# Kernel tuning notes

Measured on AMD Instinct MI355X. Metric: run time of the kernel, lower is better.

The kernel has to match this reference:

```python
import jax, jax.numpy as jnp
import numpy as np

N_NODES = 100000
N_EDGES = 500000
D_IN = 128
D_HID = 256
D_OUT = 1


def mish(x):
    # x * tanh(softplus(x))
    return x * jnp.tanh(jax.nn.softplus(x))


def setup_inputs() -> dict:
    key = jax.random.key(0)
    k1, k2, k3, k4, k5, k6 = jax.random.split(key, 6)
    z = jax.random.normal(k1, (N_NODES, D_IN), dtype=jnp.float32)
    edge = jax.random.randint(k2, (2, N_EDGES), 0, N_NODES, dtype=jnp.int64)
    # PyTorch Linear default init: U(-1/sqrt(fan_in), 1/sqrt(fan_in))
    s1 = 1.0 / np.sqrt(D_IN)
    s2 = 1.0 / np.sqrt(D_HID)
    W1 = jax.random.uniform(k3, (D_HID, D_IN), minval=-s1, maxval=s1, dtype=jnp.float32)
    b1 = jax.random.uniform(k4, (D_HID,), minval=-s1, maxval=s1, dtype=jnp.float32)
    W2 = jax.random.uniform(k5, (D_OUT, D_HID), minval=-s2, maxval=s2, dtype=jnp.float32)
    b2 = jax.random.uniform(k6, (D_OUT,), minval=-s2, maxval=s2, dtype=jnp.float32)
    return {"z": z, "edge": edge, "W1": W1, "b1": b1, "W2": W2, "b2": b2}


def reference(z, edge, W1, b1, W2, b2):
    # gather node pairs and elementwise product: [E, D_IN]
    x = z[edge[0]] * z[edge[1]]
    # fc1 + mish (dropout is identity in eval mode)
    h = mish(jnp.einsum('ed,hd->eh', x, W1) + b1)
    # fc2 + sigmoid -> [E, 1]
    logits = jnp.einsum('eh,oh->eo', h, W2) + b2
    return jax.nn.sigmoid(logits)
```

## Files before the change

kernel.cpp:

```cpp
#include <hip/hip_runtime.h>
#include <hip/hip_bf16.h>


#define N_EDGES 500000
#define D_IN    128
#define D_HID   256
#define M_TILE  32
#define NTILES  (N_EDGES / M_TILE)
#define LDS_STRIDE 136
#define GRID    1024

typedef __bf16 bf16x8 __attribute__((ext_vector_type(8)));
typedef float  f32x16 __attribute__((ext_vector_type(16)));
typedef float  f32x2  __attribute__((ext_vector_type(2)));

union F4H { float4 v; f32x2 h[2]; };

__device__ __forceinline__ unsigned int pkbf(f32x2 q) {
    union { __hip_bfloat162 b; unsigned int u; } c;
    c.b = __float22bfloat162_rn(make_float2(q.x, q.y));
    return c.u;
}

__device__ __forceinline__ f32x2 mish2(f32x2 x) {
    f32x2 xc = {fminf(x.x, 20.0f), fminf(x.y, 20.0f)};
    f32x2 E  = {__expf(xc.x), __expf(xc.y)};
    f32x2 num = E * (E + 2.0f);
    f32x2 den = num + 2.0f;
    f32x2 r  = {__builtin_amdgcn_rcpf(den.x), __builtin_amdgcn_rcpf(den.y)};
    return x * num * r;
}

__global__ __launch_bounds__(512, 2)
void edge_decoder_kernel(const float* __restrict__ z,
                         const int*   __restrict__ edge,
                         const float* __restrict__ W1,
                         const float* __restrict__ b1,
                         const float* __restrict__ W2,
                         const float* __restrict__ b2,
                         float*       __restrict__ out) {
    __shared__ ushort xbuf[2][M_TILE * LDS_STRIDE];
    __shared__ float  lpart[2][8][M_TILE];

    const int t    = threadIdx.x;
    const int wave = t >> 6;
    const int lane = t & 63;
    const int half = lane >> 5;
    const int col  = lane & 31;

    bf16x8 afragW[8];
    {
        const float* wrow = W1 + (size_t)(wave * 32 + col) * D_IN;
        #pragma unroll
        for (int kk = 0; kk < 8; ++kk) {
            const float* wp = wrow + kk * 16 + half * 8;
            F4H w0{*reinterpret_cast<const float4*>(wp)};
            F4H w1{*reinterpret_cast<const float4*>(wp + 4)};
            union { unsigned int u[4]; bf16x8 v; } o;
            o.u[0] = pkbf(w0.h[0]); o.u[1] = pkbf(w0.h[1]);
            o.u[2] = pkbf(w1.h[0]); o.u[3] = pkbf(w1.h[1]);
            afragW[kk] = o.v;
        }
    }
    float b1c[16], w2f[16];
    #pragma unroll
    for (int r = 0; r < 16; ++r) {
        const int n = wave * 32 + (r & 3) + 8 * (r >> 2) + 4 * half;
        b1c[r] = b1[n];
        w2f[r] = W2[n];
    }
    const float b2f = b2[0];

    const int s_slot = t >> 4;
    const int cch    = t & 15;

    int tile = blockIdx.x;
    float4 a0, a1, c0, c1;
    {
        const int e = tile * M_TILE + s_slot;
        const int u = edge[e], v = edge[N_EDGES + e];
        const float* zu = z + (size_t)u * D_IN + cch * 8;
        const float* zv = z + (size_t)v * D_IN + cch * 8;
        a0 = *reinterpret_cast<const float4*>(zu);
        a1 = *reinterpret_cast<const float4*>(zu + 4);
        c0 = *reinterpret_cast<const float4*>(zv);
        c1 = *reinterpret_cast<const float4*>(zv + 4);
    }
    int u_n, v_n;
    {
        const int t1 = min(tile + GRID, NTILES - 1);
        const int e1 = t1 * M_TILE + s_slot;
        u_n = edge[e1]; v_n = edge[N_EDGES + e1];
    }

    int  p = 0;
    bool have_prev = false;
    int  prev_base = 0;

    for (; tile < NTILES; tile += GRID) {
        {
            F4H A0{a0}, A1{a1}, C0{c0}, C1{c1};
            *reinterpret_cast<uint4*>(&xbuf[p][s_slot * LDS_STRIDE + cch * 8]) =
                make_uint4(pkbf(A0.h[0] * C0.h[0]), pkbf(A0.h[1] * C0.h[1]),
                           pkbf(A1.h[0] * C1.h[0]), pkbf(A1.h[1] * C1.h[1]));
        }
        __syncthreads();

        {
            const float* zu = z + (size_t)u_n * D_IN + cch * 8;
            const float* zv = z + (size_t)v_n * D_IN + cch * 8;
            a0 = *reinterpret_cast<const float4*>(zu);
            a1 = *reinterpret_cast<const float4*>(zu + 4);
            c0 = *reinterpret_cast<const float4*>(zv);
            c1 = *reinterpret_cast<const float4*>(zv + 4);
        }
        {
            const int t2 = min(tile + 2 * GRID, NTILES - 1);
            const int e2 = t2 * M_TILE + s_slot;
            u_n = edge[e2]; v_n = edge[N_EDGES + e2];
        }

        if (have_prev && t < M_TILE) {
            const int pp = p ^ 1;
            float logit = b2f;
            #pragma unroll
            for (int w = 0; w < 8; ++w) logit += lpart[pp][w][t];
            out[prev_base + t] = __builtin_amdgcn_rcpf(1.0f + __expf(-logit));
        }

        f32x16 acc;
        #pragma unroll
        for (int r = 0; r < 16; ++r) acc[r] = b1c[r];

        #pragma unroll
        for (int kk = 0; kk < 8; ++kk) {
            bf16x8 bx = *reinterpret_cast<const bf16x8*>(
                &xbuf[p][col * LDS_STRIDE + kk * 16 + half * 8]);
            acc = __builtin_amdgcn_mfma_f32_32x32x16_bf16(afragW[kk], bx, acc, 0, 0, 0);
        }

        float s = 0.f;
        #pragma unroll
        for (int r = 0; r < 16; r += 2) {
            f32x2 h = {acc[r], acc[r + 1]};
            f32x2 m = mish2(h);
            s = fmaf(m.x, w2f[r], s);
            s = fmaf(m.y, w2f[r + 1], s);
        }
        s += __shfl_xor(s, 32);
        if (lane < 32) lpart[p][wave][col] = s;

        have_prev = true;
        prev_base = tile * M_TILE;
        p ^= 1;
    }

    __syncthreads();
    if (have_prev && t < M_TILE) {
        const int pp = p ^ 1;
        float logit = b2f;
        #pragma unroll
        for (int w = 0; w < 8; ++w) logit += lpart[pp][w][t];
        out[prev_base + t] = __builtin_amdgcn_rcpf(1.0f + __expf(-logit));
    }
}

extern "C" void kernel_launch(void* const* d_in, const int* in_sizes, int n_in,
                              void* d_out, int out_size, void* d_ws, size_t ws_size,
                              hipStream_t stream) {
    const float* z    = (const float*)d_in[0];
    const int*   edge = (const int*)d_in[1];
    const float* W1   = (const float*)d_in[2];
    const float* b1   = (const float*)d_in[3];
    const float* W2   = (const float*)d_in[4];
    const float* b2   = (const float*)d_in[5];
    float* out = (float*)d_out;

    edge_decoder_kernel<<<dim3(GRID), dim3(512), 0, stream>>>(z, edge, W1, b1, W2, b2, out);
}
```

Before: 180.0 us.

## Pre-convert z to bf16 and restructure decoder into barrier-free per-wave tiles

Adds a pre-pass that converts the node feature table z to bf16 in the workspace, which halves the bytes fetched by the random gathers. The main kernel now gives each wave a whole 32-edge tile and computes all 256 hidden units itself, using W1 fragments staged in LDS with b1 folded in as an extra K-slice. This removes the block-wide __syncthreads and the LDS reduction of partial logits. The cost is an extra kernel launch, a full pass over z on every call, 8x more LDS reads of W1 per tile, and a fallback to the old kernel when the workspace is too small.

```diff
diff --git a/kernel.cpp b/kernel.cpp
--- a/kernel.cpp
+++ b/kernel.cpp
@@ -2,16 +2,17 @@
 #include <hip/hip_bf16.h>
 
 
+#define N_NODES 100000
 #define N_EDGES 500000
 #define D_IN    128
 #define D_HID   256
-#define M_TILE  32
-#define NTILES  (N_EDGES / M_TILE)
-#define LDS_STRIDE 136
-#define GRID    1024
+#define NTILES  (N_EDGES / 32)
+#define GRID    512
+#define NWAVES  (GRID * 4)
 
 typedef __bf16 bf16x8 __attribute__((ext_vector_type(8)));
 typedef float  f32x16 __attribute__((ext_vector_type(16)));
+typedef float  f32x4  __attribute__((ext_vector_type(4)));
 typedef float  f32x2  __attribute__((ext_vector_type(2)));
 
 union F4H { float4 v; f32x2 h[2]; };
@@ -21,33 +22,183 @@
     c.b = __float22bfloat162_rn(make_float2(q.x, q.y));
     return c.u;
 }
-
-__device__ __forceinline__ f32x2 mish2(f32x2 x) {
-    f32x2 xc = {fminf(x.x, 20.0f), fminf(x.y, 20.0f)};
-    f32x2 E  = {__expf(xc.x), __expf(xc.y)};
-    f32x2 num = E * (E + 2.0f);
-    f32x2 den = num + 2.0f;
-    f32x2 r  = {__builtin_amdgcn_rcpf(den.x), __builtin_amdgcn_rcpf(den.y)};
-    return x * num * r;
-}
-
-__global__ __launch_bounds__(512, 2)
-void edge_decoder_kernel(const float* __restrict__ z,
-                         const int*   __restrict__ edge,
-                         const float* __restrict__ W1,
-                         const float* __restrict__ b1,
-                         const float* __restrict__ W2,
-                         const float* __restrict__ b2,
-                         float*       __restrict__ out) {
-    __shared__ ushort xbuf[2][M_TILE * LDS_STRIDE];
-    __shared__ float  lpart[2][8][M_TILE];
+__device__ __forceinline__ unsigned short f2bf(float f) {
+    union { float f; unsigned int u; } c; c.f = f;
+    return (unsigned short)((c.u + 0x7fffu + ((c.u >> 16) & 1u)) >> 16);
+}
+__device__ __forceinline__ float bflo(unsigned int w) {
+    union { unsigned int u; float f; } c; c.u = w << 16; return c.f;
+}
+__device__ __forceinline__ float bfhi(unsigned int w) {
+    union { unsigned int u; float f; } c; c.u = w & 0xffff0000u; return c.f;
+}
+
+__device__ __forceinline__ float mish_f(float x) {
+    float xc  = fminf(x, 20.0f);
+    float E   = __expf(xc);
+    float num = E * (E + 2.0f);
+    return x * num * __builtin_amdgcn_rcpf(num + 2.0f);
+}
+
+__global__ __launch_bounds__(256)
+void z_to_bf16(const float* __restrict__ z, ushort* __restrict__ zb) {
+    const int i = (blockIdx.x * 256 + threadIdx.x) * 8;
+    F4H a{*reinterpret_cast<const float4*>(z + i)};
+    F4H b{*reinterpret_cast<const float4*>(z + i + 4)};
+    *reinterpret_cast<uint4*>(zb + i) =
+        make_uint4(pkbf(a.h[0]), pkbf(a.h[1]), pkbf(b.h[0]), pkbf(b.h[1]));
+}
+
+__global__ __launch_bounds__(256, 2)
+void edge_decoder_nobar(const ushort* __restrict__ zb,
+                        const int*    __restrict__ edge,
+                        const float*  __restrict__ W1,
+                        const float*  __restrict__ b1,
+                        const float*  __restrict__ W2,
+                        const float*  __restrict__ b2,
+                        float*        __restrict__ out) {
+    __shared__ ushort ldsA[8 * 9 * 64 * 8];
+    __shared__ float  ldsW2[D_HID];
 
     const int t    = threadIdx.x;
     const int wave = t >> 6;
     const int lane = t & 63;
+    const int ecol = lane & 31;
     const int half = lane >> 5;
-    const int col  = lane & 31;
-
+
+    ldsW2[t] = W2[t];
+    for (int c = t; c < 8 * 9 * 64; c += 256) {
+        const int ln = c & 63, mtkk = c >> 6;
+        const int mt = mtkk / 9, kk = mtkk - mt * 9;
+        const int m = mt * 32 + (ln & 31), hf = ln >> 5;
+        union { unsigned int u[4]; uint4 q; } o;
+        if (kk < 8) {
+            const float* wp = W1 + (size_t)m * D_IN + kk * 16 + hf * 8;
+            F4H w0{*reinterpret_cast<const float4*>(wp)};
+            F4H w1{*reinterpret_cast<const float4*>(wp + 4)};
+            o.u[0] = pkbf(w0.h[0]); o.u[1] = pkbf(w0.h[1]);
+            o.u[2] = pkbf(w1.h[0]); o.u[3] = pkbf(w1.h[1]);
+        } else {
+            o.u[0] = o.u[1] = o.u[2] = o.u[3] = 0u;
+            if (hf == 0) o.u[0] = (unsigned int)f2bf(b1[m]);
+        }
+        *reinterpret_cast<uint4*>(&ldsA[c * 8]) = o.q;
+    }
+    __syncthreads();
+
+    const float b2f = b2[0];
+
+    bf16x8 bfr8;
+    {
+        union { unsigned short s[8]; bf16x8 v; } u;
+        #pragma unroll
+        for (int j = 0; j < 8; ++j) u.s[j] = 0;
+        if (half == 0) u.s[0] = 0x3F80;
+        bfr8 = u.v;
+    }
+
+    int T = blockIdx.x * 4 + wave;
+    if (T >= NTILES) return;
+
+    uint4 su[8], sv[8];
+    {
+        const int e = T * 32 + ecol;
+        const int u = edge[e], v = edge[N_EDGES + e];
+        const ushort* ru = zb + (size_t)u * D_IN + half * 8;
+        const ushort* rv = zb + (size_t)v * D_IN + half * 8;
+        #pragma unroll
+        for (int kk = 0; kk < 8; ++kk) {
+            su[kk] = *reinterpret_cast<const uint4*>(ru + kk * 16);
+            sv[kk] = *reinterpret_cast<const uint4*>(rv + kk * 16);
+        }
+    }
+    int eun = 0, evn = 0;
+    {
+        const int Tn = T + NWAVES;
+        if (Tn < NTILES) {
+            const int e = Tn * 32 + ecol;
+            eun = edge[e]; evn = edge[N_EDGES + e];
+        }
+    }
+
+    while (true) {
+        bf16x8 bfr[8];
+        #pragma unroll
+        for (int kk = 0; kk < 8; ++kk) {
+            unsigned int uu[4] = {su[kk].x, su[kk].y, su[kk].z, su[kk].w};
+            unsigned int vv[4] = {sv[kk].x, sv[kk].y, sv[kk].z, sv[kk].w};
+            union { unsigned int u[4]; bf16x8 v; } o;
+            #pragma unroll
+            for (int j = 0; j < 4; ++j) {
+                f32x2 fu = {bflo(uu[j]), bfhi(uu[j])};
+                f32x2 fv = {bflo(vv[j]), bfhi(vv[j])};
+                o.u[j] = pkbf(fu * fv);
+            }
+            bfr[kk] = o.v;
+        }
+
+        const int Tn = T + NWAVES;
+        const bool hn = Tn < NTILES;
+        if (hn) {
+            const ushort* ru = zb + (size_t)eun * D_IN + half * 8;
+            const ushort* rv = zb + (size_t)evn * D_IN + half * 8;
+            #pragma unroll
+            for (int kk = 0; kk < 8; ++kk) {
+                su[kk] = *reinterpret_cast<const uint4*>(ru + kk * 16);
+                sv[kk] = *reinterpret_cast<const uint4*>(rv + kk * 16);
+            }
+            const int Tnn = Tn + NWAVES;
+            if (Tnn < NTILES) {
+                const int e = Tnn * 32 + ecol;
+                eun = edge[e]; evn = edge[N_EDGES + e];
+            }
+        }
+
+        float s = 0.f;
+        #pragma unroll
+        for (int mt = 0; mt < 8; ++mt) {
+            f32x16 acc = {0.f, 0.f, 0.f, 0.f, 0.f, 0.f, 0.f, 0.f,
+                          0.f, 0.f, 0.f, 0.f, 0.f, 0.f, 0.f, 0.f};
+            #pragma unroll
+            for (int kk = 0; kk < 9; ++kk) {
+                bf16x8 a = *reinterpret_cast<const bf16x8*>(
+                    &ldsA[((mt * 9 + kk) * 64 + lane) * 8]);
+                acc = __builtin_amdgcn_mfma_f32_32x32x16_bf16(
+                    a, (kk < 8) ? bfr[kk] : bfr8, acc, 0, 0, 0);
+            }
+            #pragma unroll
+            for (int g = 0; g < 4; ++g) {
+                f32x4 w = *reinterpret_cast<const f32x4*>(
+                    &ldsW2[mt * 32 + g * 8 + half * 4]);
+                #pragma unroll
+                for (int j = 0; j < 4; ++j)
+                    s = fmaf(mish_f(acc[g * 4 + j]), w[j], s);
+            }
+        }
+        s += __shfl_xor(s, 32);
+        if (lane < 32) {
+            const float logit = s + b2f;
+            out[T * 32 + ecol] = __builtin_amdgcn_rcpf(1.0f + __expf(-logit));
+        }
+
+        if (!hn) break;
+        T = Tn;
+    }
+}
+
+#define M_TILE  32
+#define LDS_STRIDE 136
+#define FGRID   1024
+
+__global__ __launch_bounds__(512, 2)
+void edge_decoder_fb(const float* __restrict__ z, const int* __restrict__ edge,
+                     const float* __restrict__ W1, const float* __restrict__ b1,
+                     const float* __restrict__ W2, const float* __restrict__ b2,
+                     float* __restrict__ out) {
+    __shared__ ushort xbuf[2][M_TILE * LDS_STRIDE];
+    __shared__ float  lpart[2][8][M_TILE];
+    const int t = threadIdx.x, wave = t >> 6, lane = t & 63;
+    const int half = lane >> 5, col = lane & 31;
     bf16x8 afragW[8];
     {
         const float* wrow = W1 + (size_t)(wave * 32 + col) * D_IN;
@@ -66,14 +217,10 @@
     #pragma unroll
     for (int r = 0; r < 16; ++r) {
         const int n = wave * 32 + (r & 3) + 8 * (r >> 2) + 4 * half;
-        b1c[r] = b1[n];
-        w2f[r] = W2[n];
+        b1c[r] = b1[n]; w2f[r] = W2[n];
     }
     const float b2f = b2[0];
-
-    const int s_slot = t >> 4;
-    const int cch    = t & 15;
-
+    const int s_slot = t >> 4, cch = t & 15;
     int tile = blockIdx.x;
     float4 a0, a1, c0, c1;
     {
@@ -81,23 +228,16 @@
         const int u = edge[e], v = edge[N_EDGES + e];
         const float* zu = z + (size_t)u * D_IN + cch * 8;
         const float* zv = z + (size_t)v * D_IN + cch * 8;
-        a0 = *reinterpret_cast<const float4*>(zu);
-        a1 = *reinterpret_cast<const float4*>(zu + 4);
-        c0 = *reinterpret_cast<const float4*>(zv);
-        c1 = *reinterpret_cast<const float4*>(zv + 4);
+        a0 = *reinterpret_cast<const float4*>(zu); a1 = *reinterpret_cast<const float4*>(zu + 4);
+        c0 = *reinterpret_cast<const float4*>(zv); c1 = *reinterpret_cast<const float4*>(zv + 4);
     }
     int u_n, v_n;
     {
-        const int t1 = min(tile + GRID, NTILES - 1);
-        const int e1 = t1 * M_TILE + s_slot;
-        u_n = edge[e1]; v_n = edge[N_EDGES + e1];
-    }
-
-    int  p = 0;
-    bool have_prev = false;
-    int  prev_base = 0;
-
-    for (; tile < NTILES; tile += GRID) {
+        const int t1 = min(tile + FGRID, NTILES - 1);
+        u_n = edge[t1 * M_TILE + s_slot]; v_n = edge[N_EDGES + t1 * M_TILE + s_slot];
+    }
+    int p = 0; bool have_prev = false; int prev_base = 0;
+    for (; tile < NTILES; tile += FGRID) {
         {
             F4H A0{a0}, A1{a1}, C0{c0}, C1{c1};
             *reinterpret_cast<uint4*>(&xbuf[p][s_slot * LDS_STRIDE + cch * 8]) =
@@ -105,60 +245,41 @@
                            pkbf(A1.h[0] * C1.h[0]), pkbf(A1.h[1] * C1.h[1]));
         }
         __syncthreads();
-
         {
             const float* zu = z + (size_t)u_n * D_IN + cch * 8;
             const float* zv = z + (size_t)v_n * D_IN + cch * 8;
-            a0 = *reinterpret_cast<const float4*>(zu);
-            a1 = *reinterpret_cast<const float4*>(zu + 4);
-            c0 = *reinterpret_cast<const float4*>(zv);
-            c1 = *reinterpret_cast<const float4*>(zv + 4);
+            a0 = *reinterpret_cast<const float4*>(zu); a1 = *reinterpret_cast<const float4*>(zu + 4);
+            c0 = *reinterpret_cast<const float4*>(zv); c1 = *reinterpret_cast<const float4*>(zv + 4);
         }
         {
-            const int t2 = min(tile + 2 * GRID, NTILES - 1);
-            const int e2 = t2 * M_TILE + s_slot;
-            u_n = edge[e2]; v_n = edge[N_EDGES + e2];
-        }
-
+            const int t2 = min(tile + 2 * FGRID, NTILES - 1);
+            u_n = edge[t2 * M_TILE + s_slot]; v_n = edge[N_EDGES + t2 * M_TILE + s_slot];
+        }
         if (have_prev && t < M_TILE) {
-            const int pp = p ^ 1;
-            float logit = b2f;
+            const int pp = p ^ 1; float logit = b2f;
             #pragma unroll
             for (int w = 0; w < 8; ++w) logit += lpart[pp][w][t];
             out[prev_base + t] = __builtin_amdgcn_rcpf(1.0f + __expf(-logit));
         }
-
         f32x16 acc;
         #pragma unroll
         for (int r = 0; r < 16; ++r) acc[r] = b1c[r];
-
         #pragma unroll
         for (int kk = 0; kk < 8; ++kk) {
             bf16x8 bx = *reinterpret_cast<const bf16x8*>(
                 &xbuf[p][col * LDS_STRIDE + kk * 16 + half * 8]);
             acc = __builtin_amdgcn_mfma_f32_32x32x16_bf16(afragW[kk], bx, acc, 0, 0, 0);
         }
-
         float s = 0.f;
         #pragma unroll
-        for (int r = 0; r < 16; r += 2) {
-            f32x2 h = {acc[r], acc[r + 1]};
-            f32x2 m = mish2(h);
-            s = fmaf(m.x, w2f[r], s);
-            s = fmaf(m.y, w2f[r + 1], s);
-        }
+        for (int r = 0; r < 16; ++r) s = fmaf(mish_f(acc[r]), w2f[r], s);
         s += __shfl_xor(s, 32);
         if (lane < 32) lpart[p][wave][col] = s;
-
-        have_prev = true;
-        prev_base = tile * M_TILE;
-        p ^= 1;
-    }
-
+        have_prev = true; prev_base = tile * M_TILE; p ^= 1;
+    }
     __syncthreads();
     if (have_prev && t < M_TILE) {
-        const int pp = p ^ 1;
-        float logit = b2f;
+        const int pp = p ^ 1; float logit = b2f;
         #pragma unroll
         for (int w = 0; w < 8; ++w) logit += lpart[pp][w][t];
         out[prev_base + t] = __builtin_amdgcn_rcpf(1.0f + __expf(-logit));
@@ -176,5 +297,14 @@
     const float* b2   = (const float*)d_in[5];
     float* out = (float*)d_out;
 
-    edge_decoder_kernel<<<dim3(GRID), dim3(512), 0, stream>>>(z, edge, W1, b1, W2, b2, out);
-}
+    const size_t zb_bytes = (size_t)N_NODES * D_IN * sizeof(ushort);
+    if (ws_size >= zb_bytes) {
+        ushort* zb = (ushort*)d_ws;
+        z_to_bf16<<<dim3((N_NODES * D_IN) / (256 * 8)), dim3(256), 0, stream>>>(z, zb);
+        edge_decoder_nobar<<<dim3(GRID), dim3(256), 0, stream>>>(
+            zb, edge, W1, b1, W2, b2, out);
+    } else {
+        edge_decoder_fb<<<dim3(FGRID), dim3(512), 0, stream>>>(
+            z, edge, W1, b1, W2, b2, out);
+    }
+}
```

Measured after the change: 387.3 us. 115% more time.
